# Performance work log

Measured on AMD Instinct MI355X. Metric: run time of the kernel, lower is better.

## Reference

```python
import jax, jax.numpy as jnp
import numpy as np

B, S, HID = 2, 2048, 2560
H, HKV, D = 8, 4, 256          # query heads, kv heads, head_dim
GROUPS = H // HKV
Q_SIZE, KV_SIZE = H * D, HKV * D
SLIDING_WINDOW = 512
SCALE = 256.0 ** -0.5          # query_pre_attn_scalar ** -0.5
EPS = 1e-6
ROPE_THETA = 10000.0


def setup_inputs() -> dict:
    key = jax.random.key(0)
    k1, k2, k3 = jax.random.split(key, 3)
    return {
        "hidden_states": jax.random.normal(k1, (B, S, HID), jnp.float32),
        "w_qkv": jax.random.normal(k2, (HID, Q_SIZE + 2 * KV_SIZE), jnp.float32) * (HID ** -0.5),
        "w_o": jax.random.normal(k3, (H * D, HID), jnp.float32) * ((H * D) ** -0.5),
        "q_norm_w": jnp.zeros((D,), jnp.float32),   # Gemma RMSNorm uses (1 + w)
        "k_norm_w": jnp.zeros((D,), jnp.float32),
        "positions": jnp.arange(S, dtype=jnp.int32),
    }


def _gemma_rms_norm(x, w, eps=EPS):
    # Gemma3RMSNorm: normalize in fp32, scale by (1 + w)
    xf = x.astype(jnp.float32)
    n = xf * jax.lax.rsqrt(jnp.mean(xf * xf, axis=-1, keepdims=True) + eps)
    return (n * (1.0 + w)).astype(x.dtype)


def _rope(q, k, positions):
    # q: [B,S,H,D], k: [B,S,HKV,D]; rotate_half RoPE, unsqueeze_dim=2 (head axis)
    half = D // 2
    inv_freq = 1.0 / (ROPE_THETA ** (jnp.arange(0, D, 2, dtype=jnp.float32) / D))  # [D/2]
    ang = positions.astype(jnp.float32)[:, None] * inv_freq[None, :]               # [S,D/2]
    emb = jnp.concatenate([ang, ang], axis=-1)                                     # [S,D]
    cos = jnp.cos(emb)[None, :, None, :]
    sin = jnp.sin(emb)[None, :, None, :]

    def rot(x):
        x1, x2 = x[..., :half], x[..., half:]
        return jnp.concatenate([-x2, x1], axis=-1)

    return q * cos + rot(q) * sin, k * cos + rot(k) * sin


def reference(hidden_states, w_qkv, w_o, q_norm_w, k_norm_w, positions):
    bsz, q_len, _ = hidden_states.shape
    qkv = jnp.einsum("bsh,hd->bsd", hidden_states, w_qkv)
    q, k, v = jnp.split(qkv, [Q_SIZE, Q_SIZE + KV_SIZE], axis=-1)
    Q = q.reshape(bsz, q_len, H, D)
    K = k.reshape(bsz, q_len, HKV, D)
    V = v.reshape(bsz, q_len, HKV, D)

    Q = _gemma_rms_norm(Q, q_norm_w)
    K = _gemma_rms_norm(K, k_norm_w)
    Q, K = _rope(Q, K, positions)

    # GQA: repeat kv heads to match query heads
    Kr = jnp.repeat(K, GROUPS, axis=2)  # [B,S,H,D]
    Vr = jnp.repeat(V, GROUPS, axis=2)

    scores = jnp.einsum("bqhd,bkhd->bhqk", Q, Kr) * SCALE  # [B,H,S,S]

    i = positions[:, None].astype(jnp.int32)
    j = positions[None, :].astype(jnp.int32)
    mask = (j <= i) & ((i - j) < SLIDING_WINDOW)           # causal + sliding window
    scores = jnp.where(mask[None, None, :, :], scores, jnp.float32(-1e30))

    probs = jax.nn.softmax(scores.astype(jnp.float32), axis=-1).astype(Q.dtype)
    out = jnp.einsum("bhqk,bkhd->bqhd", probs, Vr).reshape(bsz, q_len, H * D)
    return jnp.einsum("bsd,dh->bsh", out, w_o)
```

## Files before the change

kernel.cpp:

```cpp
#include <hip/hip_runtime.h>
#include <hip/hip_bf16.h>
#include <stdint.h>

#define QSCALE 0.09016844005555459f

typedef __attribute__((ext_vector_type(4))) float f32x4;
typedef __attribute__((ext_vector_type(8))) __bf16 bf16x8;
typedef __attribute__((ext_vector_type(8))) unsigned short ushort8;

static __device__ __forceinline__ float bf2f(unsigned short v) {
  union { unsigned u; float f; } x; x.u = ((unsigned)v) << 16; return x.f;
}
static __device__ __forceinline__ unsigned short f2bf(float f) {
  union { float f; unsigned u; } x; x.f = f;
  unsigned r = x.u + 0x7fffu + ((x.u >> 16) & 1u);
  return (unsigned short)(r >> 16);
}
static __device__ __forceinline__ void gload16(const void* g, void* l) {
  __builtin_amdgcn_global_load_lds((const __attribute__((address_space(1))) void*)g,
                                   (__attribute__((address_space(3))) void*)l, 16, 0, 0);
}
#define SBAR() __builtin_amdgcn_s_barrier()

__global__ __launch_bounds__(256) void k_rope_tab(const int* __restrict__ pos,
                                                  float* __restrict__ ct,
                                                  float* __restrict__ st) {
  int idx = blockIdx.x * 256 + threadIdx.x;
  int s = idx >> 7, j = idx & 127;
  float inv = exp2f((float)j * (-13.287712379549449f / 128.0f));
  float ang = (float)pos[s] * inv;
  float sv, cv;
  sincosf(ang, &sv, &cv);
  ct[idx] = cv; st[idx] = sv;
}

__global__ __launch_bounds__(256) void k_cvt_bf16(const float* __restrict__ in,
                                                  unsigned short* __restrict__ out, int n4) {
  int i = blockIdx.x * 256 + threadIdx.x;
  if (i >= n4) return;
  float4 v = ((const float4*)in)[i];
  ushort4 o; o.x = f2bf(v.x); o.y = f2bf(v.y); o.z = f2bf(v.z); o.w = f2bf(v.w);
  ((ushort4*)out)[i] = o;
}

__global__ __launch_bounds__(256) void k_transpose_w(const float* __restrict__ in,
                                                     unsigned short* __restrict__ out,
                                                     int R, int C) {
  __shared__ float tile[32][33];
  int c0 = blockIdx.x * 32, r0 = blockIdx.y * 32;
  int tx = threadIdx.x & 31, ty = threadIdx.x >> 5;
#pragma unroll
  for (int i = 0; i < 4; i++)
    tile[ty + 8*i][tx] = in[(size_t)(r0 + ty + 8*i) * C + c0 + tx];
  __syncthreads();
#pragma unroll
  for (int i = 0; i < 4; i++)
    out[(size_t)(c0 + ty + 8*i) * R + r0 + tx] = f2bf(tile[tx][ty + 8*i]);
}

template <bool F32OUT>
__global__ __launch_bounds__(512, 1) void k_gemm256(const unsigned short* __restrict__ A,
                                                    const unsigned short* __restrict__ Bt,
                                                    void* __restrict__ Cm,
                                                    int M, int N, int K) {
  __shared__ __align__(16) unsigned short ldsA[4][8192];
  __shared__ __align__(16) unsigned short ldsB[4][8192];
  const int nbn = N >> 8;
  int bid = blockIdx.x;
  int nwg = gridDim.x;
  if ((nwg & 7) == 0) {
    int cpx = nwg >> 3;
    bid = (bid & 7) * cpx + (bid >> 3);
  }
  const int bm = bid / nbn, bn = bid % nbn;
  const int tid = threadIdx.x;
  const int w = tid >> 6, l = tid & 63;
  const int wm = w >> 2, wn = w & 3;
  const int lr = l & 15, lk = l >> 4;
  const int nt = K >> 5;

  const int rL = tid >> 2;
  const int swc = ((tid & 3) ^ ((tid >> 3) & 3)) << 3;
  const unsigned short* Ag = A + (size_t)(bm * 256 + rL) * K + swc;
  const unsigned short* Bg = Bt + (size_t)(bn * 256 + rL) * K + swc;
  const int ldsoff = w * 512;
  const int wb = ((lk ^ ((lr >> 1) & 3)) << 3);
  const int arow0 = wm * 128 + lr;
  const int brow0 = wn * 64 + lr;

  f32x4 acc[8][4] = {};

#define STAGE_A(kt_, s_) do { \
    gload16(Ag + (size_t)(kt_) * 32,                    (char*)&ldsA[s_][ldsoff]); \
    gload16(Ag + (size_t)(kt_) * 32 + (size_t)128 * K,  (char*)&ldsA[s_][4096 + ldsoff]); } while (0)
#define STAGE_B(kt_, s_) do { \
    gload16(Bg + (size_t)(kt_) * 32,                    (char*)&ldsB[s_][ldsoff]); \
    gload16(Bg + (size_t)(kt_) * 32 + (size_t)128 * K,  (char*)&ldsB[s_][4096 + ldsoff]); } while (0)

#define KSTEP(kt_, S_, PF_, VMC_, TAILBAR_) do { \
    bf16x8 af[8], bf[4]; \
    _Pragma("unroll") \
    for (int i = 0; i < 8; ++i) \
      af[i] = *(const bf16x8*)&ldsA[S_][((arow0 + i * 16) << 5) + wb]; \
    _Pragma("unroll") \
    for (int j = 0; j < 4; ++j) \
      bf[j] = *(const bf16x8*)&ldsB[S_][((brow0 + j * 16) << 5) + wb]; \
    if (PF_) { STAGE_A((kt_) + 3, ((S_) + 3) & 3); STAGE_B((kt_) + 3, ((S_) + 3) & 3); } \
    __builtin_amdgcn_s_setprio(1); \
    _Pragma("unroll") \
    for (int i = 0; i < 8; ++i) \
      _Pragma("unroll") \
      for (int j = 0; j < 4; ++j) \
        acc[i][j] = __builtin_amdgcn_mfma_f32_16x16x32_bf16(af[i], bf[j], acc[i][j], 0, 0, 0); \
    __builtin_amdgcn_s_setprio(0); \
    if ((VMC_) == 8)      { asm volatile("s_waitcnt vmcnt(8)" ::: "memory"); } \
    else if ((VMC_) == 4) { asm volatile("s_waitcnt vmcnt(4)" ::: "memory"); } \
    else if ((VMC_) == 0) { asm volatile("s_waitcnt vmcnt(0)" ::: "memory"); } \
    if (TAILBAR_) SBAR(); \
  } while (0)

  STAGE_A(0, 0); STAGE_B(0, 0);
  STAGE_A(1, 1); STAGE_B(1, 1);
  STAGE_A(2, 2); STAGE_B(2, 2);
  asm volatile("s_waitcnt vmcnt(8)" ::: "memory");
  SBAR();

  const int ng = nt >> 2;
  for (int g = 0; g < ng - 1; ++g) {
    const int kt0 = g << 2;
    KSTEP(kt0 + 0, 0, true, 8, true);
    KSTEP(kt0 + 1, 1, true, 8, true);
    KSTEP(kt0 + 2, 2, true, 8, true);
    KSTEP(kt0 + 3, 3, true, 8, true);
  }
  {
    const int kt0 = nt - 4;
    KSTEP(kt0 + 0, 0, true, 8, true);
    KSTEP(kt0 + 1, 1, false, 4, true);
    KSTEP(kt0 + 2, 2, false, 0, true);
    KSTEP(kt0 + 3, 3, false, -1, false);
  }
#undef KSTEP
#undef STAGE_A
#undef STAGE_B

#pragma unroll
  for (int i = 0; i < 8; ++i)
#pragma unroll
    for (int j = 0; j < 4; ++j) {
      int row = bm * 256 + wm * 128 + i * 16 + lk * 4;
      int col = bn * 256 + wn * 64 + j * 16 + lr;
#pragma unroll
      for (int r = 0; r < 4; ++r) {
        if constexpr (F32OUT)
          ((float*)Cm)[(size_t)(row + r) * N + col] = acc[i][j][r];
        else
          ((unsigned short*)Cm)[(size_t)(row + r) * N + col] = f2bf(acc[i][j][r]);
      }
    }
}

__global__ __launch_bounds__(256) void k_norm_rope(
    const unsigned short* __restrict__ qkv,
    const float* __restrict__ qw, const float* __restrict__ kw,
    const float* __restrict__ ct, const float* __restrict__ st,
    unsigned short* __restrict__ Qh, unsigned short* __restrict__ Kh) {
  int gwid = (blockIdx.x * 256 + threadIdx.x) >> 6;
  int l = threadIdx.x & 63;
  int head = gwid % 12;
  int bs = gwid / 12;
  int b = bs >> 11, s = bs & 2047;
  bool isq = head < 8;
  int col = isq ? head * 256 : 2048 + (head - 8) * 256;
  const unsigned short* src = qkv + (size_t)bs * 4096 + col;
  int d0 = l * 4;
  ushort4 u = *(const ushort4*)(src + d0);
  float x0 = bf2f(u.x), x1 = bf2f(u.y), x2 = bf2f(u.z), x3 = bf2f(u.w);
  float ss = x0 * x0 + x1 * x1 + x2 * x2 + x3 * x3;
#pragma unroll
  for (int off = 32; off > 0; off >>= 1) ss += __shfl_xor(ss, off);
  float inv = rsqrtf(ss * (1.0f / 256.0f) + 1e-6f);
  const float* wv = isq ? qw : kw;
  float4 w4 = *(const float4*)(wv + d0);
  float y0 = x0 * inv * (1.0f + w4.x);
  float y1 = x1 * inv * (1.0f + w4.y);
  float y2 = x2 * inv * (1.0f + w4.z);
  float y3 = x3 * inv * (1.0f + w4.w);
  int fb = (l & 31) * 4;
  float4 c4 = *(const float4*)(ct + s * 128 + fb);
  float4 s4 = *(const float4*)(st + s * 128 + fb);
  float p0 = __shfl_xor(y0, 32), p1 = __shfl_xor(y1, 32);
  float p2 = __shfl_xor(y2, 32), p3 = __shfl_xor(y3, 32);
  float sg = (l < 32) ? -1.0f : 1.0f;
  float o0 = y0 * c4.x + sg * p0 * s4.x;
  float o1 = y1 * c4.y + sg * p1 * s4.y;
  float o2 = y2 * c4.z + sg * p2 * s4.z;
  float o3 = y3 * c4.w + sg * p3 * s4.w;
  if (isq) {
    o0 *= QSCALE; o1 *= QSCALE; o2 *= QSCALE; o3 *= QSCALE;
    unsigned short* dst = Qh + (((size_t)(b * 8 + head)) * 2048 + s) * 256 + d0;
    ushort4 o; o.x = f2bf(o0); o.y = f2bf(o1); o.z = f2bf(o2); o.w = f2bf(o3);
    *(ushort4*)dst = o;
  } else {
    int hk = head - 8;
    int ch = d0 >> 3;
    int dsw = ((ch ^ (s & 7)) << 3) | (d0 & 7);
    unsigned short* dst = Kh + (((size_t)(b * 4 + hk)) * 2048 + s) * 256 + dsw;
    ushort4 o; o.x = f2bf(o0); o.y = f2bf(o1); o.z = f2bf(o2); o.w = f2bf(o3);
    *(ushort4*)dst = o;
  }
}

__global__ __launch_bounds__(256) void k_vtrans(const unsigned short* __restrict__ qkv,
                                                unsigned short* __restrict__ VT) {
  __shared__ __align__(16) unsigned short tile[64][72];
  int bid = blockIdx.x;
  int dt = bid & 3, stile = (bid >> 2) & 31, hk = (bid >> 7) & 3, b = bid >> 9;
  int s0 = stile * 64, d0 = dt * 64;
  int t = threadIdx.x;
#pragma unroll
  for (int i = 0; i < 2; i++) {
    int flat = i * 256 + t;
    int sl = flat >> 3, dc = flat & 7;
    ushort8 v = *(const ushort8*)&qkv[(size_t)(b * 2048 + s0 + sl) * 4096 + 3072 + hk * 256 + d0 + dc * 8];
    *(ushort8*)&tile[sl][dc * 8] = v;
  }
  __syncthreads();
#pragma unroll
  for (int i = 0; i < 2; i++) {
    int flat = i * 256 + t;
    int dl = flat >> 3, sc = flat & 7;
    ushort8 v;
#pragma unroll
    for (int j = 0; j < 8; j++) v[j] = tile[sc * 8 + j][dl];
    int dg = d0 + dl;
    int chg = (s0 >> 3) + sc;
    int swc = chg ^ (dg & 7);
    *(ushort8*)&VT[((size_t)(b * 4 + hk) * 256 + dg) * 2048 + swc * 8] = v;
  }
}

__global__ __launch_bounds__(512) void k_attn(
    const unsigned short* __restrict__ Qh,
    const unsigned short* __restrict__ Kh,
    const unsigned short* __restrict__ VT,
    const int* __restrict__ pos,
    unsigned short* __restrict__ Ao) {
  __shared__ __align__(16) unsigned short Ks[64 * 256];
  __shared__ __align__(16) unsigned short Vs[256 * 64];
  __shared__ __align__(16) unsigned short Ps[8][16 * 72];
  int bid = blockIdx.x;
  int qt = bid & 31, hk = (bid >> 5) & 3, b = bid >> 7;
  int t = threadIdx.x, w = t >> 6, l = t & 63;
  int lr = l & 15, lk = l >> 4;
  int h = hk * 2 + (w >> 2);
  int q0 = qt * 64, qrow0 = q0 + (w & 3) * 16;
  const unsigned short* qbase = Qh + (((size_t)(b * 8 + h)) * 2048 + (qrow0 + lr)) * 256;
  bf16x8 qf[8];
#pragma unroll
  for (int c = 0; c < 8; c++) qf[c] = *(const bf16x8*)&qbase[c * 32 + lk * 8];
  int pq[4];
#pragma unroll
  for (int r = 0; r < 4; r++) pq[r] = pos[qrow0 + lk * 4 + r];
  float m[4], ll[4];
  f32x4 oacc[16];
  f32x4 zero4 = {0.f, 0.f, 0.f, 0.f};
#pragma unroll
  for (int r = 0; r < 4; r++) { m[r] = -1e30f; ll[r] = 0.0f; }
#pragma unroll
  for (int nd = 0; nd < 16; nd++) oacc[nd] = zero4;
  const char* Kbase = (const char*)(Kh + ((size_t)(b * 4 + hk)) * 2048 * 256);
  const char* Vbase = (const char*)(VT + ((size_t)(b * 4 + hk)) * 256 * 2048);
  int jlo = q0 - 511; if (jlo < 0) jlo = 0; jlo &= ~63;
  for (int j0 = jlo; j0 < q0 + 64; j0 += 64) {
#pragma unroll
    for (int i = 0; i < 4; i++)
      gload16(Kbase + (size_t)j0 * 512 + i * 8192 + t * 16, (char*)Ks + i * 8192 + w * 1024);
#pragma unroll
    for (int i = 0; i < 4; i++) {
      int off = i * 8192 + t * 16;
      int d = off >> 7, rb = off & 127;
      gload16(Vbase + (size_t)d * 4096 + j0 * 2 + rb, (char*)Vs + i * 8192 + w * 1024);
    }
    __syncthreads();
    f32x4 sacc[4];
#pragma unroll
    for (int n = 0; n < 4; n++) sacc[n] = zero4;
#pragma unroll
    for (int n = 0; n < 4; n++) {
      int key = n * 16 + lr;
      int sw = (key & 7) << 4;
#pragma unroll
      for (int c = 0; c < 8; c++) {
        bf16x8 kf = *(const bf16x8*)((const char*)Ks + key * 512 + ((c * 64 + lk * 16) ^ sw));
        sacc[n] = __builtin_amdgcn_mfma_f32_16x16x32_bf16(qf[c], kf, sacc[n], 0, 0, 0);
      }
    }
    int pk[4];
#pragma unroll
    for (int n = 0; n < 4; n++) pk[n] = pos[j0 + n * 16 + lr];
#pragma unroll
    for (int n = 0; n < 4; n++)
#pragma unroll
      for (int r = 0; r < 4; r++) {
        int dq = pq[r] - pk[n];
        if (!(dq >= 0 && dq < 512)) sacc[n][r] = -1e30f;
      }
    float tm[4], rs[4], mn[4], corr[4];
#pragma unroll
    for (int r = 0; r < 4; r++)
      tm[r] = fmaxf(fmaxf(sacc[0][r], sacc[1][r]), fmaxf(sacc[2][r], sacc[3][r]));
#pragma unroll
    for (int d = 1; d < 16; d <<= 1)
#pragma unroll
      for (int r = 0; r < 4; r++) tm[r] = fmaxf(tm[r], __shfl_xor(tm[r], d));
#pragma unroll
    for (int r = 0; r < 4; r++) {
      mn[r] = fmaxf(m[r], tm[r]);
      corr[r] = exp2f(m[r] - mn[r]);
      rs[r] = 0.f;
    }
#pragma unroll
    for (int n = 0; n < 4; n++)
#pragma unroll
      for (int r = 0; r < 4; r++) {
        float sv = sacc[n][r];
        float p = (sv > -1e29f) ? exp2f(sv - mn[r]) : 0.0f;
        sacc[n][r] = p;
        rs[r] += p;
      }
#pragma unroll
    for (int d = 1; d < 16; d <<= 1)
#pragma unroll
      for (int r = 0; r < 4; r++) rs[r] += __shfl_xor(rs[r], d);
#pragma unroll
    for (int r = 0; r < 4; r++) { ll[r] = ll[r] * corr[r] + rs[r]; m[r] = mn[r]; }
#pragma unroll
    for (int nd = 0; nd < 16; nd++)
#pragma unroll
      for (int r = 0; r < 4; r++) oacc[nd][r] *= corr[r];
#pragma unroll
    for (int n = 0; n < 4; n++)
#pragma unroll
      for (int r = 0; r < 4; r++)
        Ps[w][(lk * 4 + r) * 72 + n * 16 + lr] = f2bf(sacc[n][r]);
#pragma unroll
    for (int c2 = 0; c2 < 2; c2++) {
      bf16x8 pf = *(const bf16x8*)&Ps[w][lr * 72 + c2 * 32 + lk * 8];
#pragma unroll
      for (int nd = 0; nd < 16; nd++) {
        int dr = nd * 16 + lr;
        bf16x8 vf = *(const bf16x8*)((const char*)Vs + dr * 128 + ((c2 * 64 + lk * 16) ^ ((dr & 7) << 4)));
        oacc[nd] = __builtin_amdgcn_mfma_f32_16x16x32_bf16(pf, vf, oacc[nd], 0, 0, 0);
      }
    }
    __syncthreads();
  }
#pragma unroll
  for (int r = 0; r < 4; r++) ll[r] = 1.0f / ll[r];
#pragma unroll
  for (int nd = 0; nd < 16; nd++)
#pragma unroll
    for (int r = 0; r < 4; r++) {
      float v = oacc[nd][r] * ll[r];
      Ao[((size_t)(b * 2048 + qrow0 + lk * 4 + r)) * 2048 + h * 256 + nd * 16 + lr] = f2bf(v);
    }
}

extern "C" void kernel_launch(void* const* d_in, const int* in_sizes, int n_in,
                              void* d_out, int out_size, void* d_ws, size_t ws_size,
                              hipStream_t stream) {
  const float* hs   = (const float*)d_in[0];
  const float* wqkv = (const float*)d_in[1];
  const float* wo   = (const float*)d_in[2];
  const float* qnw  = (const float*)d_in[3];
  const float* knw  = (const float*)d_in[4];
  const int*   pos  = (const int*)d_in[5];
  float* out = (float*)d_out;

  char* base = (char*)d_ws;
  const size_t OFF_R0 = 0;
  const size_t OFF_R1 = 33554432;
  const size_t OFF_R2 = 54525952;
  const size_t OFF_R3 = 75497472;

  unsigned short* QKV = (unsigned short*)(base + OFF_R0);
  unsigned short* Ao  = (unsigned short*)(base + OFF_R0);
  unsigned short* WoT = (unsigned short*)(base + OFF_R0 + 16777216);
  unsigned short* Xb  = (unsigned short*)(base + OFF_R1);
  unsigned short* Qh  = (unsigned short*)(base + OFF_R1);
  unsigned short* WqT = (unsigned short*)(base + OFF_R2);
  unsigned short* Kh  = (unsigned short*)(base + OFF_R2);
  unsigned short* VT  = (unsigned short*)(base + OFF_R2 + 8388608);
  float* ct = (float*)(base + OFF_R3);
  float* st = (float*)(base + OFF_R3 + 1048576);

  k_rope_tab<<<1024, 256, 0, stream>>>(pos, ct, st);
  k_cvt_bf16<<<10240, 256, 0, stream>>>(hs, Xb, 2621440);
  k_transpose_w<<<dim3(128, 80), 256, 0, stream>>>(wqkv, WqT, 2560, 4096);
  k_gemm256<false><<<256, 512, 0, stream>>>(Xb, WqT, QKV, 4096, 4096, 2560);
  k_norm_rope<<<12288, 256, 0, stream>>>(QKV, qnw, knw, ct, st, Qh, Kh);
  k_vtrans<<<1024, 256, 0, stream>>>(QKV, VT);
  k_transpose_w<<<dim3(80, 64), 256, 0, stream>>>(wo, WoT, 2048, 2560);
  k_attn<<<256, 512, 0, stream>>>(Qh, Kh, VT, pos, Ao);
  k_gemm256<true><<<160, 512, 0, stream>>>(Ao, WoT, out, 4096, 2560, 2048);
}
```

Before: 236.1 us.

## Double-buffer K/V tiles in attention kernel with async prefetch

The attention kernel now keeps two LDS buffers for the K and V tiles and issues the global-to-LDS loads for the next key tile before computing on the current one. It waits with a partial vmcnt so only the current tile's loads must land, which lets the memory latency overlap with the MFMA work. It also raises wave priority around the MFMA loops. LDS use doubles to about 144KB per block, which may limit occupancy. The partial vmcnt wait relies on the exact count of outstanding loads, and the raw s_barrier may not cover LDS write visibility the way __syncthreads did.

```diff
diff --git a/kernel.cpp b/kernel.cpp
--- a/kernel.cpp
+++ b/kernel.cpp
@@ -246,8 +246,8 @@
     const unsigned short* __restrict__ VT,
     const int* __restrict__ pos,
     unsigned short* __restrict__ Ao) {
-  __shared__ __align__(16) unsigned short Ks[64 * 256];
-  __shared__ __align__(16) unsigned short Vs[256 * 64];
+  __shared__ __align__(16) unsigned short Ks[2][64 * 256];
+  __shared__ __align__(16) unsigned short Vs[2][256 * 64];
   __shared__ __align__(16) unsigned short Ps[8][16 * 72];
   int bid = blockIdx.x;
   int qt = bid & 31, hk = (bid >> 5) & 3, b = bid >> 7;
@@ -272,30 +272,50 @@
   const char* Kbase = (const char*)(Kh + ((size_t)(b * 4 + hk)) * 2048 * 256);
   const char* Vbase = (const char*)(VT + ((size_t)(b * 4 + hk)) * 256 * 2048);
   int jlo = q0 - 511; if (jlo < 0) jlo = 0; jlo &= ~63;
-  for (int j0 = jlo; j0 < q0 + 64; j0 += 64) {
-#pragma unroll
-    for (int i = 0; i < 4; i++)
-      gload16(Kbase + (size_t)j0 * 512 + i * 8192 + t * 16, (char*)Ks + i * 8192 + w * 1024);
-#pragma unroll
-    for (int i = 0; i < 4; i++) {
-      int off = i * 8192 + t * 16;
-      int d = off >> 7, rb = off & 127;
-      gload16(Vbase + (size_t)d * 4096 + j0 * 2 + rb, (char*)Vs + i * 8192 + w * 1024);
-    }
-    __syncthreads();
+  const int ntj = ((q0 + 64) - jlo) >> 6;
+
+#define ASTAGE(tj_) do { \
+    const int j0_ = jlo + (tj_) * 64; \
+    char* kd_ = (char*)Ks[(tj_) & 1]; \
+    char* vd_ = (char*)Vs[(tj_) & 1]; \
+    _Pragma("unroll") \
+    for (int i = 0; i < 4; i++) \
+      gload16(Kbase + (size_t)j0_ * 512 + i * 8192 + t * 16, kd_ + i * 8192 + w * 1024); \
+    _Pragma("unroll") \
+    for (int i = 0; i < 4; i++) { \
+      int off_ = i * 8192 + t * 16; \
+      int d_ = off_ >> 7, rb_ = off_ & 127; \
+      gload16(Vbase + (size_t)d_ * 4096 + j0_ * 2 + rb_, vd_ + i * 8192 + w * 1024); \
+    } \
+  } while (0)
+
+  ASTAGE(0);
+  for (int tj = 0; tj < ntj; ++tj) {
+    const int j0 = jlo + tj * 64;
+    const char* Kb = (const char*)Ks[tj & 1];
+    const char* Vb = (const char*)Vs[tj & 1];
+    if (tj + 1 < ntj) {
+      ASTAGE(tj + 1);
+      asm volatile("s_waitcnt vmcnt(8)" ::: "memory");
+    } else {
+      asm volatile("s_waitcnt vmcnt(0)" ::: "memory");
+    }
+    SBAR();
     f32x4 sacc[4];
 #pragma unroll
     for (int n = 0; n < 4; n++) sacc[n] = zero4;
+    __builtin_amdgcn_s_setprio(1);
 #pragma unroll
     for (int n = 0; n < 4; n++) {
       int key = n * 16 + lr;
       int sw = (key & 7) << 4;
 #pragma unroll
       for (int c = 0; c < 8; c++) {
-        bf16x8 kf = *(const bf16x8*)((const char*)Ks + key * 512 + ((c * 64 + lk * 16) ^ sw));
+        bf16x8 kf = *(const bf16x8*)(Kb + key * 512 + ((c * 64 + lk * 16) ^ sw));
         sacc[n] = __builtin_amdgcn_mfma_f32_16x16x32_bf16(qf[c], kf, sacc[n], 0, 0, 0);
       }
     }
+    __builtin_amdgcn_s_setprio(0);
     int pk[4];
 #pragma unroll
     for (int n = 0; n < 4; n++) pk[n] = pos[j0 + n * 16 + lr];
@@ -347,15 +367,18 @@
 #pragma unroll
     for (int c2 = 0; c2 < 2; c2++) {
       bf16x8 pf = *(const bf16x8*)&Ps[w][lr * 72 + c2 * 32 + lk * 8];
+      __builtin_amdgcn_s_setprio(1);
 #pragma unroll
       for (int nd = 0; nd < 16; nd++) {
         int dr = nd * 16 + lr;
-        bf16x8 vf = *(const bf16x8*)((const char*)Vs + dr * 128 + ((c2 * 64 + lk * 16) ^ ((dr & 7) << 4)));
+        bf16x8 vf = *(const bf16x8*)(Vb + dr * 128 + ((c2 * 64 + lk * 16) ^ ((dr & 7) << 4)));
         oacc[nd] = __builtin_amdgcn_mfma_f32_16x16x32_bf16(pf, vf, oacc[nd], 0, 0, 0);
       }
-    }
-    __syncthreads();
-  }
+      __builtin_amdgcn_s_setprio(0);
+    }
+    SBAR();
+  }
+#undef ASTAGE
 #pragma unroll
   for (int r = 0; r < 4; r++) ll[r] = 1.0f / ll[r];
 #pragma unroll
```

Measured after the change: 232.4 us. Within noise of the previous version (-1.6%).
